# Kernel tuning notes

Measured on AMD Instinct MI355X. Metric: run time of the kernel, lower is better.

The kernel has to match this reference:

```python
import jax, jax.numpy as jnp
import numpy as np

BETA = 0.25  # commitment cost (original code's undefined self.betas)


def setup_inputs() -> dict:
    key = jax.random.key(0)
    k1, k2 = jax.random.split(key)
    B, D, H, W = 32, 256, 32, 32
    K = 1024
    x = jax.random.normal(k1, (B, D, H, W), dtype=jnp.float32)
    # nn.Embedding init: uniform(-1/K, 1/K)
    emb = jax.random.uniform(k2, (K, D), dtype=jnp.float32,
                             minval=-1.0 / K, maxval=1.0 / K)
    return {"x": x, "emb": emb}


def reference(x, emb):
    # x: [B, D, H, W] -> NHWC
    xp = jnp.transpose(x, (0, 2, 3, 1))          # [B, H, W, D]
    D = emb.shape[1]
    z = xp.reshape(-1, D)                        # [N, D]
    # pairwise squared distance: ||z||^2 + ||e||^2 - 2 z e^T
    dist = (jnp.sum(z * z, axis=1, keepdims=True)
            + jnp.sum(emb * emb, axis=1)
            - 2.0 * jnp.einsum('nd,kd->nk', z, emb))  # [N, K]
    idx = jnp.argmin(dist, axis=1)               # [N] int
    z_quant = emb[idx].reshape(xp.shape)         # [B, H, W, D]
    sg = jax.lax.stop_gradient
    loss = (jnp.mean((sg(z_quant) - xp) ** 2)
            + BETA * jnp.mean((z_quant - sg(xp)) ** 2))
    # straight-through estimator
    z_quant = xp + sg(z_quant - xp)
    z_quant = jnp.transpose(z_quant, (0, 3, 1, 2))  # back to NCHW
    return z_quant, idx, loss
```

## Files before the change

kernel.cpp:

```cpp
#include <hip/hip_runtime.h>

typedef _Float16 half8 __attribute__((ext_vector_type(8)));
typedef _Float16 half4v __attribute__((ext_vector_type(4)));
typedef float f32x4 __attribute__((ext_vector_type(4)));

#define ZQ_ELEMS 8388608
#define N_TOK    32768
#define D_DIM    256
#define K_CB     1024

#define FLAG_CAP 8192
#define ESCALE   1024.0f
#define TAU      0.15f

__device__ __align__(16) _Float16 g_eh[K_CB * D_DIM];
__device__ __align__(16) float g_ebT[D_DIM * K_CB];
__device__ float g_ck[K_CB];
__device__ float g_bk[K_CB];
__device__ float g_loss;
__device__ int   g_cnt;
__device__ int   g_flags[FLAG_CAP];
__device__ float g_zst[FLAG_CAP * 256];
__device__ float g_aA[FLAG_CAP];
__device__ unsigned long long g_best[FLAG_CAP];

__device__ __forceinline__ unsigned long long enc_dk(float D, int k) {
  unsigned int b = __float_as_uint(D);
  unsigned int u = (b & 0x80000000u) ? ~b : (b | 0x80000000u);
  return (((unsigned long long)u) << 32) | (unsigned int)k;
}

__global__ __launch_bounds__(256) void vq_prep(const float* __restrict__ emb) {
  const int tid = threadIdx.x;
  const int w   = tid >> 6;
  const int l   = tid & 63;
  const int k   = (blockIdx.x << 2) + w;
  f32x4 v = *(const f32x4*)(emb + (k << 8) + (l << 2));
  double sd = (double)v[0]*v[0] + (double)v[1]*v[1] + (double)v[2]*v[2] + (double)v[3]*v[3];
  #pragma unroll
  for (int m = 1; m < 64; m <<= 1) sd += __shfl_xor(sd, m);
  if (l == 0) { g_bk[k] = (float)sd; g_ck[k] = 512.0f * (float)sd; }
  half4v h;
  h[0] = (_Float16)(v[0] * ESCALE); h[1] = (_Float16)(v[1] * ESCALE);
  h[2] = (_Float16)(v[2] * ESCALE); h[3] = (_Float16)(v[3] * ESCALE);
  *(half4v*)(g_eh + (k << 8) + (l << 2)) = h;
  const int gi = blockIdx.x * 256 + tid;
  if (gi < FLAG_CAP) g_best[gi] = ~0ULL;
  if (blockIdx.x == 0 && tid == 0) { g_loss = 0.0f; g_cnt = 0; }
}

__global__ __launch_bounds__(256) void vq_tr(const float* __restrict__ emb) {
  __shared__ float tl[64][65];
  const int tx = threadIdx.x & 63, ty = threadIdx.x >> 6;
  const int k0 = (blockIdx.x & 15) << 6;
  const int d0 = (blockIdx.x >> 4) << 6;
  #pragma unroll
  for (int j = 0; j < 16; j++) {
    const int kk = (ty << 4) + j;
    tl[kk][tx] = emb[((k0 + kk) << 8) + d0 + tx];
  }
  __syncthreads();
  #pragma unroll
  for (int j = 0; j < 16; j++) {
    const int dd = (ty << 4) + j;
    g_ebT[((d0 + dd) << 10) + k0 + tx] = tl[tx][dd];
  }
}

__global__ __launch_bounds__(256, 2) void vq_main(const float* __restrict__ x,
                                                  const float* __restrict__ emb,
                                                  float* __restrict__ out) {
  __shared__ __align__(16) _Float16 zt[64 * 256];
  __shared__ float ckl[K_CB];
  __shared__ float wv1[4][64], wv2[4][64];
  __shared__ int   wi1[4][64];
  __shared__ int   fidx[64];
  __shared__ float lred[4];

  const int tid = threadIdx.x;
  const int n0  = blockIdx.x * 64;
  const int b   = blockIdx.x >> 4;
  const int hw0 = (blockIdx.x & 15) << 6;

  #pragma unroll
  for (int i = 0; i < 4; i++) ckl[tid + 256 * i] = g_ck[tid + 256 * i];

  {
    const int hw8 = (tid & 7) << 3;
    const int dl  = tid >> 3;
    #pragma unroll
    for (int it = 0; it < 8; it++) {
      const int d = (it << 5) + dl;
      const float* src = x + (((b << 8) + d) << 10) + hw0 + hw8;
      f32x4 a0 = *(const f32x4*)src;
      f32x4 a1 = *(const f32x4*)(src + 4);
      _Float16 cv[8];
      cv[0]=(_Float16)a0[0]; cv[1]=(_Float16)a0[1]; cv[2]=(_Float16)a0[2]; cv[3]=(_Float16)a0[3];
      cv[4]=(_Float16)a1[0]; cv[5]=(_Float16)a1[1]; cv[6]=(_Float16)a1[2]; cv[7]=(_Float16)a1[3];
      const int blkx = d >> 3;
      #pragma unroll
      for (int i = 0; i < 8; i++) {
        const int n   = hw8 + i;
        const int blk = blkx ^ i ^ (tid & 7);
        zt[(n << 8) + (blk << 3) + (d & 7)] = cv[i];
      }
    }
  }
  __syncthreads();

  const int w = tid >> 6;
  const int l = tid & 63;
  const int c = l & 15;
  const int q = l >> 4;

  half8 af[4][8];
  #pragma unroll
  for (int t = 0; t < 4; t++) {
    const int n  = (t << 4) + c;
    const int sw = (n & 7) ^ (n >> 3);
    #pragma unroll
    for (int s = 0; s < 8; s++) {
      const int K = (s << 2) + q;
      af[t][s] = *(const half8*)(zt + (n << 8) + ((K ^ sw) << 3));
    }
  }

  float v1[4][4], v2[4][4]; int i1[4][4];
  #pragma unroll
  for (int t = 0; t < 4; t++)
    #pragma unroll
    for (int r = 0; r < 4; r++) { v1[t][r] = -3e38f; v2[t][r] = -3e38f; i1[t][r] = 0; }

  for (int jj = 0; jj < 16; jj++) {
    const int k0 = (w << 4) + (jj << 6);
    const float ckv = ckl[k0 + c];
    f32x4 acc[4];
    #pragma unroll
    for (int t = 0; t < 4; t++) acc[t] = f32x4{-ckv, -ckv, -ckv, -ckv};
    #pragma unroll
    for (int s = 0; s < 8; s++) {
      const half8 bf = *(const half8*)(g_eh + ((k0 + c) << 8) + (s << 5) + (q << 3));
      #pragma unroll
      for (int t = 0; t < 4; t++)
        acc[t] = __builtin_amdgcn_mfma_f32_16x16x32_f16(af[t][s], bf, acc[t], 0, 0, 0);
    }
    const int kk = k0 + c;
    #pragma unroll
    for (int t = 0; t < 4; t++)
      #pragma unroll
      for (int r = 0; r < 4; r++) {
        const float sv = acc[t][r];
        if (sv > v1[t][r]) { v2[t][r] = v1[t][r]; v1[t][r] = sv; i1[t][r] = kk; }
        else if (sv > v2[t][r]) v2[t][r] = sv;
      }
  }

  #pragma unroll
  for (int t = 0; t < 4; t++)
    #pragma unroll
    for (int r = 0; r < 4; r++) {
      float a1v = v1[t][r], a2v = v2[t][r]; int ai = i1[t][r];
      #pragma unroll
      for (int m = 8; m >= 1; m >>= 1) {
        const float o1 = __shfl_xor(a1v, m);
        const int   oi = __shfl_xor(ai, m);
        const float o2 = __shfl_xor(a2v, m);
        if (o1 > a1v || (o1 == a1v && oi < ai)) { a2v = fmaxf(a1v, o2); a1v = o1; ai = oi; }
        else a2v = fmaxf(a2v, o1);
      }
      if (c == 0) {
        const int nl = (t << 4) + (q << 2) + r;
        wv1[w][nl] = a1v; wv2[w][nl] = a2v; wi1[w][nl] = ai;
      }
    }
  __syncthreads();

  if (tid < 64) {
    float a1v = wv1[0][tid], a2v = wv2[0][tid]; int ai = wi1[0][tid];
    #pragma unroll
    for (int ww = 1; ww < 4; ww++) {
      const float o1 = wv1[ww][tid]; const int oi = wi1[ww][tid]; const float o2 = wv2[ww][tid];
      if (o1 > a1v || (o1 == a1v && oi < ai)) { a2v = fmaxf(a1v, o2); a1v = o1; ai = oi; }
      else a2v = fmaxf(a2v, o1);
    }
    fidx[tid] = ai;
    out[ZQ_ELEMS + n0 + tid] = (float)ai;
    if (a1v - a2v < TAU) {
      int p = atomicAdd(&g_cnt, 1);
      if (p < FLAG_CAP) g_flags[p] = n0 + tid;
    }
  }
  __syncthreads();

  float lacc = 0.0f;
  {
    const int hw = tid & 63;
    const int sw = (hw & 7) ^ (hw >> 3);
    const float* erow = emb + (fidx[hw] << 8);
    #pragma unroll
    for (int it = 0; it < 8; it++) {
      const int dblk = (it << 2) + w;
      half8 zv = *(const half8*)(zt + (hw << 8) + ((dblk ^ sw) << 3));
      f32x4 e0 = *(const f32x4*)(erow + (dblk << 3));
      f32x4 e1 = *(const f32x4*)(erow + (dblk << 3) + 4);
      #pragma unroll
      for (int j = 0; j < 8; j++) {
        const int d = (dblk << 3) + j;
        const float ef = (j < 4) ? e0[j] : e1[j - 4];
        const float df = ef - (float)zv[j];
        lacc += df * df;
        out[(((b << 8) + d) << 10) + hw0 + hw] = ef;
      }
    }
  }
  #pragma unroll
  for (int m = 1; m < 64; m <<= 1) lacc += __shfl_xor(lacc, m);
  if (l == 0) lred[w] = lacc;
  __syncthreads();
  if (tid == 0) atomicAdd(&g_loss, lred[0] + lred[1] + lred[2] + lred[3]);
}

__global__ __launch_bounds__(256) void vq_stage(const float* __restrict__ x) {
  __shared__ float zl[256];
  const int tid = threadIdx.x;
  int cnt = g_cnt; if (cnt > FLAG_CAP) cnt = FLAG_CAP;
  for (int s = blockIdx.x; s < cnt; s += gridDim.x) {
    const int n = g_flags[s], b = n >> 10, hw = n & 1023;
    const float zv = x[(((b << 8) + tid) << 10) + hw];
    g_zst[(s << 8) + tid] = zv;
    zl[tid] = zv;
    __syncthreads();
    if (tid < 32) {
      double sa = 0.0;
      #pragma unroll
      for (int j = 0; j < 8; j++) { const double z = (double)zl[(tid << 3) + j]; sa += z * z; }
      #pragma unroll
      for (int m = 1; m < 32; m <<= 1) sa += __shfl_xor(sa, m);
      if (tid == 0) g_aA[s] = (float)sa;
    }
    __syncthreads();
  }
}

__global__ __launch_bounds__(256) void vq_fix() {
  __shared__ float z0l[256], z1l[256];
  __shared__ float bvv[2][256];
  __shared__ int   bkk[2][256];
  const int tid = threadIdx.x;
  int cnt = g_cnt; if (cnt > FLAG_CAP) cnt = FLAG_CAP;
  const int njob = ((cnt + 1) >> 1) << 2;
  for (int j = blockIdx.x; j < njob; j += gridDim.x) {
    const int pr = j >> 2, r = j & 3;
    const int s0 = pr << 1;
    const int s1 = (s0 + 1 < cnt) ? s0 + 1 : cnt - 1;
    z0l[tid] = g_zst[(s0 << 8) + tid];
    z1l[tid] = g_zst[(s1 << 8) + tid];
    __syncthreads();
    double c0 = 0.0, c1 = 0.0;
    const float* colbase = g_ebT + (r << 8) + tid;
    #pragma unroll 8
    for (int d = 0; d < 256; d++) {
      const double e = (double)colbase[d << 10];
      c0 = fma(e, (double)z0l[d], c0);
      c1 = fma(e, (double)z1l[d], c1);
    }
    const int k = (r << 8) + tid;
    const float bkv = g_bk[k];
    bvv[0][tid] = (g_aA[s0] + bkv) - 2.0f * (float)c0;
    bkk[0][tid] = k;
    bvv[1][tid] = (g_aA[s1] + bkv) - 2.0f * (float)c1;
    bkk[1][tid] = k;
    __syncthreads();
    for (int off = 128; off >= 1; off >>= 1) {
      if (tid < off) {
        #pragma unroll
        for (int g = 0; g < 2; g++) {
          const float v2c = bvv[g][tid + off]; const int k2 = bkk[g][tid + off];
          if (v2c < bvv[g][tid] || (v2c == bvv[g][tid] && k2 < bkk[g][tid])) {
            bvv[g][tid] = v2c; bkk[g][tid] = k2;
          }
        }
      }
      __syncthreads();
    }
    if (tid == 0) {
      atomicMin(&g_best[s0], enc_dk(bvv[0][0], bkk[0][0]));
      atomicMin(&g_best[s1], enc_dk(bvv[1][0], bkk[1][0]));
    }
    __syncthreads();
  }
}

__global__ __launch_bounds__(256) void vq_out(float* __restrict__ out) {
  int cnt = g_cnt; if (cnt > FLAG_CAP) cnt = FLAG_CAP;
  for (int s = blockIdx.x * 256 + threadIdx.x; s < cnt; s += gridDim.x * 256)
    out[ZQ_ELEMS + g_flags[s]] = (float)(unsigned int)(g_best[s] & 0xFFFFFFFFu);
}

__global__ void vq_fin(float* __restrict__ out) {
  out[ZQ_ELEMS + N_TOK] = g_loss * (1.25f / 8388608.0f);
}

extern "C" void kernel_launch(void* const* d_in, const int* in_sizes, int n_in,
                              void* d_out, int out_size, void* d_ws, size_t ws_size,
                              hipStream_t stream) {
  const float* x   = (const float*)d_in[0];
  const float* emb = (const float*)d_in[1];
  float* out = (float*)d_out;
  vq_prep<<<256, 256, 0, stream>>>(emb);
  vq_tr<<<64, 256, 0, stream>>>(emb);
  vq_main<<<512, 256, 0, stream>>>(x, emb, out);
  vq_stage<<<1024, 256, 0, stream>>>(x);
  vq_fix<<<2048, 256, 0, stream>>>();
  vq_out<<<32, 256, 0, stream>>>(out);
  vq_fin<<<1, 1, 0, stream>>>(out);
}
```

Measured before the change: 198.3 us.

## Fuse prep kernels, widen main kernel to 512 threads, pack index into score bits

Merges the norm/fp16 prep and transpose kernels into one launch, and folds the final loss write into the output-fix kernel, removing two launches. The main kernel moves to 512 threads (8 waves), each wave handling 128 codes with two B tiles per step. The A fragments are now read from LDS inside the loop instead of being held in registers. Argmin tracking packs the code index into the low 10 mantissa bits of the score, so top-2 tracking reduces to fmed3/fmax with no separate index registers or branches. This lowers register pressure and raises occupancy, but it slightly perturbs scores and adds LDS traffic; the near-tie fallback path is relied on to keep results correct.

```diff
diff --git a/kernel.cpp b/kernel.cpp
--- a/kernel.cpp
+++ b/kernel.cpp
@@ -30,67 +30,66 @@
   return (((unsigned long long)u) << 32) | (unsigned int)k;
 }
 
-__global__ __launch_bounds__(256) void vq_prep(const float* __restrict__ emb) {
+__global__ __launch_bounds__(256) void vq_prep_tr(const float* __restrict__ emb) {
+  __shared__ float tl[64][65];
   const int tid = threadIdx.x;
-  const int w   = tid >> 6;
-  const int l   = tid & 63;
-  const int k   = (blockIdx.x << 2) + w;
-  f32x4 v = *(const f32x4*)(emb + (k << 8) + (l << 2));
-  double sd = (double)v[0]*v[0] + (double)v[1]*v[1] + (double)v[2]*v[2] + (double)v[3]*v[3];
-  #pragma unroll
-  for (int m = 1; m < 64; m <<= 1) sd += __shfl_xor(sd, m);
-  if (l == 0) { g_bk[k] = (float)sd; g_ck[k] = 512.0f * (float)sd; }
-  half4v h;
-  h[0] = (_Float16)(v[0] * ESCALE); h[1] = (_Float16)(v[1] * ESCALE);
-  h[2] = (_Float16)(v[2] * ESCALE); h[3] = (_Float16)(v[3] * ESCALE);
-  *(half4v*)(g_eh + (k << 8) + (l << 2)) = h;
-  const int gi = blockIdx.x * 256 + tid;
-  if (gi < FLAG_CAP) g_best[gi] = ~0ULL;
-  if (blockIdx.x == 0 && tid == 0) { g_loss = 0.0f; g_cnt = 0; }
-}
-
-__global__ __launch_bounds__(256) void vq_tr(const float* __restrict__ emb) {
-  __shared__ float tl[64][65];
-  const int tx = threadIdx.x & 63, ty = threadIdx.x >> 6;
-  const int k0 = (blockIdx.x & 15) << 6;
-  const int d0 = (blockIdx.x >> 4) << 6;
-  #pragma unroll
-  for (int j = 0; j < 16; j++) {
-    const int kk = (ty << 4) + j;
-    tl[kk][tx] = emb[((k0 + kk) << 8) + d0 + tx];
-  }
-  __syncthreads();
-  #pragma unroll
-  for (int j = 0; j < 16; j++) {
-    const int dd = (ty << 4) + j;
-    g_ebT[((d0 + dd) << 10) + k0 + tx] = tl[tx][dd];
-  }
-}
-
-__global__ __launch_bounds__(256, 2) void vq_main(const float* __restrict__ x,
+  if (blockIdx.x < 256) {
+    const int w = tid >> 6, l = tid & 63;
+    const int k = (blockIdx.x << 2) + w;
+    f32x4 v = *(const f32x4*)(emb + (k << 8) + (l << 2));
+    double sd = (double)v[0]*v[0] + (double)v[1]*v[1] + (double)v[2]*v[2] + (double)v[3]*v[3];
+    #pragma unroll
+    for (int m = 1; m < 64; m <<= 1) sd += __shfl_xor(sd, m);
+    if (l == 0) { g_bk[k] = (float)sd; g_ck[k] = 512.0f * (float)sd; }
+    half4v h;
+    h[0] = (_Float16)(v[0] * ESCALE); h[1] = (_Float16)(v[1] * ESCALE);
+    h[2] = (_Float16)(v[2] * ESCALE); h[3] = (_Float16)(v[3] * ESCALE);
+    *(half4v*)(g_eh + (k << 8) + (l << 2)) = h;
+    const int gi = blockIdx.x * 256 + tid;
+    if (gi < FLAG_CAP) g_best[gi] = ~0ULL;
+    if (blockIdx.x == 0 && tid == 0) { g_loss = 0.0f; g_cnt = 0; }
+  } else {
+    const int bid = blockIdx.x - 256;
+    const int tx = tid & 63, ty = tid >> 6;
+    const int k0 = (bid & 15) << 6;
+    const int d0 = (bid >> 4) << 6;
+    #pragma unroll
+    for (int j = 0; j < 16; j++) {
+      const int kk = (ty << 4) + j;
+      tl[kk][tx] = emb[((k0 + kk) << 8) + d0 + tx];
+    }
+    __syncthreads();
+    #pragma unroll
+    for (int j = 0; j < 16; j++) {
+      const int dd = (ty << 4) + j;
+      g_ebT[((d0 + dd) << 10) + k0 + tx] = tl[tx][dd];
+    }
+  }
+}
+
+__global__ __launch_bounds__(512, 4) void vq_main(const float* __restrict__ x,
                                                   const float* __restrict__ emb,
                                                   float* __restrict__ out) {
   __shared__ __align__(16) _Float16 zt[64 * 256];
   __shared__ float ckl[K_CB];
-  __shared__ float wv1[4][64], wv2[4][64];
-  __shared__ int   wi1[4][64];
+  __shared__ float wv1[8][64], wv2[8][64];
   __shared__ int   fidx[64];
-  __shared__ float lred[4];
+  __shared__ float lred[8];
 
   const int tid = threadIdx.x;
   const int n0  = blockIdx.x * 64;
   const int b   = blockIdx.x >> 4;
   const int hw0 = (blockIdx.x & 15) << 6;
 
-  #pragma unroll
-  for (int i = 0; i < 4; i++) ckl[tid + 256 * i] = g_ck[tid + 256 * i];
+  ckl[tid] = g_ck[tid];
+  ckl[tid + 512] = g_ck[tid + 512];
 
   {
     const int hw8 = (tid & 7) << 3;
     const int dl  = tid >> 3;
     #pragma unroll
-    for (int it = 0; it < 8; it++) {
-      const int d = (it << 5) + dl;
+    for (int it = 0; it < 4; it++) {
+      const int d = (it << 6) + dl;
       const float* src = x + (((b << 8) + d) << 10) + hw0 + hw8;
       f32x4 a0 = *(const f32x4*)src;
       f32x4 a1 = *(const f32x4*)(src + 4);
@@ -113,79 +112,81 @@
   const int c = l & 15;
   const int q = l >> 4;
 
-  half8 af[4][8];
-  #pragma unroll
-  for (int t = 0; t < 4; t++) {
-    const int n  = (t << 4) + c;
-    const int sw = (n & 7) ^ (n >> 3);
-    #pragma unroll
-    for (int s = 0; s < 8; s++) {
-      const int K = (s << 2) + q;
-      af[t][s] = *(const half8*)(zt + (n << 8) + ((K ^ sw) << 3));
-    }
-  }
-
-  float v1[4][4], v2[4][4]; int i1[4][4];
+  float v1[4][4], v2[4][4];
   #pragma unroll
   for (int t = 0; t < 4; t++)
     #pragma unroll
-    for (int r = 0; r < 4; r++) { v1[t][r] = -3e38f; v2[t][r] = -3e38f; i1[t][r] = 0; }
-
-  for (int jj = 0; jj < 16; jj++) {
-    const int k0 = (w << 4) + (jj << 6);
-    const float ckv = ckl[k0 + c];
-    f32x4 acc[4];
-    #pragma unroll
-    for (int t = 0; t < 4; t++) acc[t] = f32x4{-ckv, -ckv, -ckv, -ckv};
+    for (int r = 0; r < 4; r++) { v1[t][r] = -3.0e38f; v2[t][r] = -3.0e38f; }
+
+  #pragma unroll 1
+  for (int mac = 0; mac < 4; mac++) {
+    const int base = (w << 7) + (mac << 5);
+    const float ck0 = ckl[base + c];
+    const float ck1 = ckl[base + 16 + c];
+    f32x4 acc[4][2];
+    #pragma unroll
+    for (int t = 0; t < 4; t++) {
+      acc[t][0] = f32x4{-ck0, -ck0, -ck0, -ck0};
+      acc[t][1] = f32x4{-ck1, -ck1, -ck1, -ck1};
+    }
     #pragma unroll
     for (int s = 0; s < 8; s++) {
-      const half8 bf = *(const half8*)(g_eh + ((k0 + c) << 8) + (s << 5) + (q << 3));
-      #pragma unroll
-      for (int t = 0; t < 4; t++)
-        acc[t] = __builtin_amdgcn_mfma_f32_16x16x32_f16(af[t][s], bf, acc[t], 0, 0, 0);
-    }
-    const int kk = k0 + c;
+      const half8 b0 = *(const half8*)(g_eh + ((base + c) << 8) + (s << 5) + (q << 3));
+      const half8 b1 = *(const half8*)(g_eh + ((base + 16 + c) << 8) + (s << 5) + (q << 3));
+      #pragma unroll
+      for (int t = 0; t < 4; t++) {
+        const int n  = (t << 4) + c;
+        const int sw = (n & 7) ^ (n >> 3);
+        const half8 a = *(const half8*)(zt + (n << 8) + ((((s << 2) + q) ^ sw) << 3));
+        acc[t][0] = __builtin_amdgcn_mfma_f32_16x16x32_f16(a, b0, acc[t][0], 0, 0, 0);
+        acc[t][1] = __builtin_amdgcn_mfma_f32_16x16x32_f16(a, b1, acc[t][1], 0, 0, 0);
+      }
+    }
     #pragma unroll
     for (int t = 0; t < 4; t++)
       #pragma unroll
-      for (int r = 0; r < 4; r++) {
-        const float sv = acc[t][r];
-        if (sv > v1[t][r]) { v2[t][r] = v1[t][r]; v1[t][r] = sv; i1[t][r] = kk; }
-        else if (sv > v2[t][r]) v2[t][r] = sv;
-      }
+      for (int r = 0; r < 4; r++)
+        #pragma unroll
+        for (int kc = 0; kc < 2; kc++) {
+          const unsigned kk = (unsigned)(base + (kc << 4) + c);
+          const unsigned su = (__float_as_uint(acc[t][kc][r]) & 0xFFFFFC00u) | kk;
+          const float se = __uint_as_float(su);
+          v2[t][r] = __builtin_amdgcn_fmed3f(se, v1[t][r], v2[t][r]);
+          v1[t][r] = fmaxf(se, v1[t][r]);
+        }
   }
 
   #pragma unroll
   for (int t = 0; t < 4; t++)
     #pragma unroll
     for (int r = 0; r < 4; r++) {
-      float a1v = v1[t][r], a2v = v2[t][r]; int ai = i1[t][r];
-      #pragma unroll
-      for (int m = 8; m >= 1; m >>= 1) {
-        const float o1 = __shfl_xor(a1v, m);
-        const int   oi = __shfl_xor(ai, m);
-        const float o2 = __shfl_xor(a2v, m);
-        if (o1 > a1v || (o1 == a1v && oi < ai)) { a2v = fmaxf(a1v, o2); a1v = o1; ai = oi; }
-        else a2v = fmaxf(a2v, o1);
+      float a1 = v1[t][r], a2 = v2[t][r];
+      #pragma unroll
+      for (int m = 1; m < 16; m <<= 1) {
+        const float o1 = __shfl_xor(a1, m);
+        const float o2 = __shfl_xor(a2, m);
+        a2 = fmaxf(fminf(a1, o1), fmaxf(a2, o2));
+        a1 = fmaxf(a1, o1);
       }
       if (c == 0) {
         const int nl = (t << 4) + (q << 2) + r;
-        wv1[w][nl] = a1v; wv2[w][nl] = a2v; wi1[w][nl] = ai;
+        wv1[w][nl] = a1; wv2[w][nl] = a2;
       }
     }
   __syncthreads();
 
   if (tid < 64) {
-    float a1v = wv1[0][tid], a2v = wv2[0][tid]; int ai = wi1[0][tid];
-    #pragma unroll
-    for (int ww = 1; ww < 4; ww++) {
-      const float o1 = wv1[ww][tid]; const int oi = wi1[ww][tid]; const float o2 = wv2[ww][tid];
-      if (o1 > a1v || (o1 == a1v && oi < ai)) { a2v = fmaxf(a1v, o2); a1v = o1; ai = oi; }
-      else a2v = fmaxf(a2v, o1);
-    }
-    fidx[tid] = ai;
-    out[ZQ_ELEMS + n0 + tid] = (float)ai;
-    if (a1v - a2v < TAU) {
+    float a1 = wv1[0][tid], a2 = wv2[0][tid];
+    #pragma unroll
+    for (int ww = 1; ww < 8; ww++) {
+      const float o1 = wv1[ww][tid], o2 = wv2[ww][tid];
+      a2 = fmaxf(fminf(a1, o1), fmaxf(a2, o2));
+      a1 = fmaxf(a1, o1);
+    }
+    const int ki = (int)(__float_as_uint(a1) & 1023u);
+    fidx[tid] = ki;
+    out[ZQ_ELEMS + n0 + tid] = (float)ki;
+    if (a1 - a2 < TAU) {
       int p = atomicAdd(&g_cnt, 1);
       if (p < FLAG_CAP) g_flags[p] = n0 + tid;
     }
@@ -194,12 +195,12 @@
 
   float lacc = 0.0f;
   {
-    const int hw = tid & 63;
+    const int hw = l;
     const int sw = (hw & 7) ^ (hw >> 3);
     const float* erow = emb + (fidx[hw] << 8);
     #pragma unroll
-    for (int it = 0; it < 8; it++) {
-      const int dblk = (it << 2) + w;
+    for (int it = 0; it < 4; it++) {
+      const int dblk = (it << 3) + w;
       half8 zv = *(const half8*)(zt + (hw << 8) + ((dblk ^ sw) << 3));
       f32x4 e0 = *(const f32x4*)(erow + (dblk << 3));
       f32x4 e1 = *(const f32x4*)(erow + (dblk << 3) + 4);
@@ -217,7 +218,12 @@
   for (int m = 1; m < 64; m <<= 1) lacc += __shfl_xor(lacc, m);
   if (l == 0) lred[w] = lacc;
   __syncthreads();
-  if (tid == 0) atomicAdd(&g_loss, lred[0] + lred[1] + lred[2] + lred[3]);
+  if (tid == 0) {
+    float s = 0.0f;
+    #pragma unroll
+    for (int ww = 0; ww < 8; ww++) s += lred[ww];
+    atomicAdd(&g_loss, s);
+  }
 }
 
 __global__ __launch_bounds__(256) void vq_stage(const float* __restrict__ x) {
@@ -291,14 +297,12 @@
   }
 }
 
-__global__ __launch_bounds__(256) void vq_out(float* __restrict__ out) {
+__global__ __launch_bounds__(256) void vq_outfin(float* __restrict__ out) {
   int cnt = g_cnt; if (cnt > FLAG_CAP) cnt = FLAG_CAP;
   for (int s = blockIdx.x * 256 + threadIdx.x; s < cnt; s += gridDim.x * 256)
     out[ZQ_ELEMS + g_flags[s]] = (float)(unsigned int)(g_best[s] & 0xFFFFFFFFu);
-}
-
-__global__ void vq_fin(float* __restrict__ out) {
-  out[ZQ_ELEMS + N_TOK] = g_loss * (1.25f / 8388608.0f);
+  if (blockIdx.x == 0 && threadIdx.x == 0)
+    out[ZQ_ELEMS + N_TOK] = g_loss * (1.25f / 8388608.0f);
 }
 
 extern "C" void kernel_launch(void* const* d_in, const int* in_sizes, int n_in,
@@ -307,11 +311,9 @@
   const float* x   = (const float*)d_in[0];
   const float* emb = (const float*)d_in[1];
   float* out = (float*)d_out;
-  vq_prep<<<256, 256, 0, stream>>>(emb);
-  vq_tr<<<64, 256, 0, stream>>>(emb);
-  vq_main<<<512, 256, 0, stream>>>(x, emb, out);
+  vq_prep_tr<<<320, 256, 0, stream>>>(emb);
+  vq_main<<<512, 512, 0, stream>>>(x, emb, out);
   vq_stage<<<1024, 256, 0, stream>>>(x);
   vq_fix<<<2048, 256, 0, stream>>>();
-  vq_out<<<32, 256, 0, stream>>>(out);
-  vq_fin<<<1, 1, 0, stream>>>(out);
-}
+  vq_outfin<<<32, 256, 0, stream>>>(out);
+}
```

Measured after the change: 251.6 us. 1.27x slower.
